# Performance work log

Hardware: AMD Instinct MI355X
Metric: run time of the kernel (lower is better)

Reference implementation:

```python
import jax, jax.numpy as jnp
import numpy as np

N_NODES = 50000
N_EDGES = 1600000
N_EDGE_F = 128
GLOBAL_F = 64
N_GRAPHS = 512
HIDDEN = N_EDGE_F // 2


def setup_inputs() -> dict:
    key = jax.random.key(0)
    k = jax.random.split(key, 8)
    x = jax.random.normal(k[0], (N_NODES, N_EDGE_F), dtype=jnp.float32)
    edge_index = jax.random.randint(k[1], (2, N_EDGES), 0, N_NODES, dtype=jnp.int64)
    edge_attr = jax.random.normal(k[2], (N_EDGES, N_EDGE_F), dtype=jnp.float32)
    u = jax.random.normal(k[3], (N_GRAPHS, GLOBAL_F), dtype=jnp.float32)
    batch = jnp.sort(jax.random.randint(k[4], (N_NODES,), 0, N_GRAPHS, dtype=jnp.int64))
    # MLP params (Linear1: in=n_edge_f+global_f, out=hidden; Linear2: hidden -> global_f)
    in1 = N_EDGE_F + GLOBAL_F
    W1 = jax.random.normal(k[5], (in1, HIDDEN), dtype=jnp.float32) / np.sqrt(in1)
    b1 = jnp.zeros((HIDDEN,), dtype=jnp.float32)
    W2 = jax.random.normal(k[6], (HIDDEN, GLOBAL_F), dtype=jnp.float32) / np.sqrt(HIDDEN)
    b2 = jnp.zeros((GLOBAL_F,), dtype=jnp.float32)
    return {"x": x, "edge_index": edge_index, "edge_attr": edge_attr, "u": u,
            "batch": batch, "W1": W1, "b1": b1, "W2": W2, "b2": b2}


def reference(x, edge_index, edge_attr, u, batch, W1, b1, W2, b2):
    # graph id of each edge = graph id of its source node
    seg = batch[edge_index[0]]                                   # [E]
    sums = jax.ops.segment_sum(edge_attr, seg, num_segments=N_GRAPHS)  # [B, n_edge_f]
    counts = jax.ops.segment_sum(jnp.ones((edge_attr.shape[0],), edge_attr.dtype),
                                 seg, num_segments=N_GRAPHS)
    mean = sums / jnp.maximum(counts, 1.0)[:, None]              # scatter-mean (0 for empty)
    out = jnp.concatenate([u, mean], axis=1)                     # [B, global_f + n_edge_f]
    # dropout in eval mode == identity
    h = jax.nn.relu(out @ W1 + b1)
    return h @ W2 + b2
```

## Files before the change

kernel.cpp:

```cpp
#include <hip/hip_runtime.h>
#include <hip/hip_bf16.h>

using u32 = unsigned int;
using u16 = unsigned short;

#define NGR   512
#define NF    128
#define GF    64
#define HID   64
#define IN1   192
#define SPLIT 8

#define HT    256
#define ITEMS 10
#define EPB   (HT * ITEMS)

__global__ void zero_counts_kernel(u32* __restrict__ counts) {
    counts[threadIdx.x] = 0u;
}

__global__ void hist_kernel(const int* __restrict__ ei0,
                            const int* __restrict__ batch,
                            u32* __restrict__ g_counts,
                            u16* __restrict__ seg, int E) {
    __shared__ u32 h[NGR];
    int tid = threadIdx.x;
    h[tid] = 0u; h[tid + 256] = 0u;
    __syncthreads();
    int base = blockIdx.x * EPB + tid;
#pragma unroll
    for (int i = 0; i < ITEMS; ++i) {
        int e = base + i * HT;
        if (e < E) {
            int s = batch[ei0[e]];
            seg[e] = (u16)s;
            atomicAdd(&h[s], 1u);
        }
    }
    __syncthreads();
    u32 v0 = h[tid];       if (v0) atomicAdd(&g_counts[tid], v0);
    u32 v1 = h[tid + 256]; if (v1) atomicAdd(&g_counts[tid + 256], v1);
}

__global__ void scan_kernel(const u32* __restrict__ counts,
                            u32* __restrict__ offsets,
                            u32* __restrict__ cursor) {
    __shared__ u32 A[NGR], B[NGR];
    int t = threadIdx.x;
    u32 c = counts[t];
    A[t] = c;
    __syncthreads();
    u32* src = A; u32* dst = B;
    for (int off = 1; off < NGR; off <<= 1) {
        u32 v = src[t];
        if (t >= off) v += src[t - off];
        dst[t] = v;
        __syncthreads();
        u32* tmp = src; src = dst; dst = tmp;
    }
    u32 exc = src[t] - c;
    offsets[t] = exc;
    cursor[t]  = exc;
}

__global__ void scatter_kernel(const u16* __restrict__ seg,
                               u32* __restrict__ cursor,
                               u32* __restrict__ sorted, int E) {
    __shared__ u32 h[NGR];
    __shared__ u32 bs[NGR];
    int tid = threadIdx.x;
    h[tid] = 0u; h[tid + 256] = 0u;
    __syncthreads();
    int base = blockIdx.x * EPB + tid;
    u16 segs[ITEMS];
    u16 ranks[ITEMS];
#pragma unroll
    for (int i = 0; i < ITEMS; ++i) {
        int e = base + i * HT;
        if (e < E) {
            int s = seg[e];
            segs[i]  = (u16)s;
            ranks[i] = (u16)atomicAdd(&h[s], 1u);
        }
    }
    __syncthreads();
    u32 v0 = h[tid];       if (v0) bs[tid]       = atomicAdd(&cursor[tid], v0);
    u32 v1 = h[tid + 256]; if (v1) bs[tid + 256] = atomicAdd(&cursor[tid + 256], v1);
    __syncthreads();
#pragma unroll
    for (int i = 0; i < ITEMS; ++i) {
        int e = base + i * HT;
        if (e < E) {
            sorted[bs[segs[i]] + ranks[i]] = (u32)e;
        }
    }
}

__launch_bounds__(256, 8)
__global__ void reduce_kernel(const float* __restrict__ edge_attr,
                              const u32* __restrict__ sorted,
                              const u32* __restrict__ counts,
                              const u32* __restrict__ offsets,
                              float* __restrict__ partial) {
    __shared__ float red[8 * NF];
    int tid = threadIdx.x;
    int g   = blockIdx.x >> 3;
    int s   = blockIdx.x & (SPLIT - 1);
    u32 off = offsets[g];
    u32 cnt = counts[g];
    u32 chunk = (cnt + SPLIT - 1) / SPLIT;
    u32 start = (u32)s * chunk;
    u32 end   = min(cnt, start + chunk);

    int row  = tid >> 5;
    int lane = tid & 31;

    float4 a0 = make_float4(0.f, 0.f, 0.f, 0.f);
    float4 a1 = a0, a2 = a0, a3 = a0;

    u32 j = start + (u32)row;
    for (; j + 24 < end; j += 32) {
        u32 e0 = sorted[off + j];
        u32 e1 = sorted[off + j + 8];
        u32 e2 = sorted[off + j + 16];
        u32 e3 = sorted[off + j + 24];
        float4 v0 = ((const float4*)(edge_attr + (size_t)e0 * NF))[lane];
        float4 v1 = ((const float4*)(edge_attr + (size_t)e1 * NF))[lane];
        float4 v2 = ((const float4*)(edge_attr + (size_t)e2 * NF))[lane];
        float4 v3 = ((const float4*)(edge_attr + (size_t)e3 * NF))[lane];
        a0.x += v0.x; a0.y += v0.y; a0.z += v0.z; a0.w += v0.w;
        a1.x += v1.x; a1.y += v1.y; a1.z += v1.z; a1.w += v1.w;
        a2.x += v2.x; a2.y += v2.y; a2.z += v2.z; a2.w += v2.w;
        a3.x += v3.x; a3.y += v3.y; a3.z += v3.z; a3.w += v3.w;
    }
    for (; j < end; j += 8) {
        u32 e = sorted[off + j];
        float4 v = ((const float4*)(edge_attr + (size_t)e * NF))[lane];
        a0.x += v.x; a0.y += v.y; a0.z += v.z; a0.w += v.w;
    }
    a0.x += a1.x + a2.x + a3.x;
    a0.y += a1.y + a2.y + a3.y;
    a0.z += a1.z + a2.z + a3.z;
    a0.w += a1.w + a2.w + a3.w;
    ((float4*)red)[row * 32 + lane] = a0;
    __syncthreads();

    if (tid < NF) {
        float v = 0.f;
#pragma unroll
        for (int r = 0; r < 8; ++r) v += red[r * NF + tid];
        partial[(size_t)blockIdx.x * NF + tid] = v;
    }
}

__global__ void final_kernel(const float* __restrict__ partial,
                             const u32* __restrict__ counts,
                             const float* __restrict__ u,
                             const float* __restrict__ W1,
                             const float* __restrict__ b1,
                             const float* __restrict__ W2,
                             const float* __restrict__ b2,
                             float* __restrict__ out) {
    __shared__ float vin[IN1];
    __shared__ float hv[HID];
    int b = blockIdx.x, t = threadIdx.x;
    if (t < NF) {
        float s = 0.f;
#pragma unroll
        for (int r = 0; r < SPLIT; ++r)
            s += partial[(size_t)(b * SPLIT + r) * NF + t];
        vin[GF + t] = s / fmaxf((float)counts[b], 1.0f);
    }
    if (t < GF) vin[t] = u[b * GF + t];
    __syncthreads();
    if (t < HID) {
        float acc = b1[t];
#pragma unroll
        for (int k = 0; k < IN1; ++k) acc += vin[k] * W1[k * HID + t];
        hv[t] = fmaxf(acc, 0.0f);
    }
    __syncthreads();
    if (t < GF) {
        float acc = b2[t];
#pragma unroll
        for (int k = 0; k < HID; ++k) acc += hv[k] * W2[k * GF + t];
        out[b * GF + t] = acc;
    }
}

extern "C" void kernel_launch(void* const* d_in, const int* in_sizes, int n_in,
                              void* d_out, int out_size, void* d_ws, size_t ws_size,
                              hipStream_t stream) {
    const int*   ei        = (const int*)d_in[1];
    const float* edge_attr = (const float*)d_in[2];
    const float* u         = (const float*)d_in[3];
    const int*   batch     = (const int*)d_in[4];
    const float* W1        = (const float*)d_in[5];
    const float* b1        = (const float*)d_in[6];
    const float* W2        = (const float*)d_in[7];
    const float* b2        = (const float*)d_in[8];
    float*       out       = (float*)d_out;

    const int E = in_sizes[1] / 2;
    const int* ei0 = ei;

    u32*   sorted  = (u32*)d_ws;
    float* partial = (float*)(sorted + E);
    u32*   counts  = (u32*)(partial + (size_t)NGR * SPLIT * NF);
    u32*   offsets = counts + NGR;
    u32*   cursor  = offsets + NGR;
    u16*   seg     = (u16*)(cursor + NGR);

    const int nblocks = (E + EPB - 1) / EPB;

    zero_counts_kernel<<<1, NGR, 0, stream>>>(counts);
    hist_kernel<<<nblocks, HT, 0, stream>>>(ei0, batch, counts, seg, E);
    scan_kernel<<<1, NGR, 0, stream>>>(counts, offsets, cursor);
    scatter_kernel<<<nblocks, HT, 0, stream>>>(seg, cursor, sorted, E);
    reduce_kernel<<<NGR * SPLIT, 256, 0, stream>>>(edge_attr, sorted, counts,
                                                   offsets, partial);
    final_kernel<<<NGR, 128, 0, stream>>>(partial, counts, u, W1, b1, W2, b2, out);
}
```

Measured before the change: 214.0 us.

## Balance reduce work with fixed-size chunk work list and nontemporal loads

Replaces the fixed 8-way split per graph with a work list built in the scan kernel, where each item covers up to 1024 sorted edges. The reduce grid is a fixed-size launch that exits early past the item count, and the final kernel sums a variable number of partials per graph. Edge attribute loads become nontemporal vector loads so the streamed rows do not pollute cache. This aims to balance load across blocks, since graph sizes vary. The cost is a serial work-list write in the scan kernel and a hard MAXIT cap that could overflow if there are many items.

```diff
diff --git a/kernel.cpp b/kernel.cpp
--- a/kernel.cpp
+++ b/kernel.cpp
@@ -1,15 +1,17 @@
 #include <hip/hip_runtime.h>
 #include <hip/hip_bf16.h>
 
-using u32 = unsigned int;
-using u16 = unsigned short;
+typedef unsigned int u32;
+typedef unsigned short u16;
+typedef float f32x4 __attribute__((ext_vector_type(4)));
 
 #define NGR   512
 #define NF    128
 #define GF    64
 #define HID   64
 #define IN1   192
-#define SPLIT 8
+#define CHUNK 1024
+#define MAXIT 2600
 
 #define HT    256
 #define ITEMS 10
@@ -44,13 +46,16 @@
 
 __global__ void scan_kernel(const u32* __restrict__ counts,
                             u32* __restrict__ offsets,
-                            u32* __restrict__ cursor) {
+                            u32* __restrict__ cursor,
+                            u32* __restrict__ work,
+                            u32* __restrict__ item_start,
+                            u32* __restrict__ header) {
     __shared__ u32 A[NGR], B[NGR];
     int t = threadIdx.x;
     u32 c = counts[t];
     A[t] = c;
     __syncthreads();
-    u32* src = A; u32* dst = B;
+    u32 *src = A, *dst = B;
     for (int off = 1; off < NGR; off <<= 1) {
         u32 v = src[t];
         if (t >= off) v += src[t - off];
@@ -61,6 +66,22 @@
     u32 exc = src[t] - c;
     offsets[t] = exc;
     cursor[t]  = exc;
+    __syncthreads();
+    u32 ns = (c + CHUNK - 1) / CHUNK;
+    A[t] = ns;
+    __syncthreads();
+    src = A; dst = B;
+    for (int off = 1; off < NGR; off <<= 1) {
+        u32 v = src[t];
+        if (t >= off) v += src[t - off];
+        dst[t] = v;
+        __syncthreads();
+        u32* tmp = src; src = dst; dst = tmp;
+    }
+    u32 istart = src[t] - ns;
+    item_start[t] = istart;
+    if (t == NGR - 1) { item_start[NGR] = istart + ns; header[0] = istart + ns; }
+    for (u32 s = 0; s < ns; ++s) work[istart + s] = ((u32)t << 16) | s;
 }
 
 __global__ void scatter_kernel(const u16* __restrict__ seg,
@@ -90,9 +111,7 @@
 #pragma unroll
     for (int i = 0; i < ITEMS; ++i) {
         int e = base + i * HT;
-        if (e < E) {
-            sorted[bs[segs[i]] + ranks[i]] = (u32)e;
-        }
+        if (e < E) sorted[bs[segs[i]] + ranks[i]] = (u32)e;
     }
 }
 
@@ -101,60 +120,57 @@
                               const u32* __restrict__ sorted,
                               const u32* __restrict__ counts,
                               const u32* __restrict__ offsets,
+                              const u32* __restrict__ work,
+                              const u32* __restrict__ header,
                               float* __restrict__ partial) {
+    const u32 id = blockIdx.x;
+    if (id >= header[0]) return;
     __shared__ float red[8 * NF];
-    int tid = threadIdx.x;
-    int g   = blockIdx.x >> 3;
-    int s   = blockIdx.x & (SPLIT - 1);
-    u32 off = offsets[g];
-    u32 cnt = counts[g];
-    u32 chunk = (cnt + SPLIT - 1) / SPLIT;
-    u32 start = (u32)s * chunk;
-    u32 end   = min(cnt, start + chunk);
-
-    int row  = tid >> 5;
-    int lane = tid & 31;
-
-    float4 a0 = make_float4(0.f, 0.f, 0.f, 0.f);
-    float4 a1 = a0, a2 = a0, a3 = a0;
-
-    u32 j = start + (u32)row;
-    for (; j + 24 < end; j += 32) {
+
+    const u32 w = work[id];
+    const int g = (int)(w >> 16);
+    const u32 sl = w & 0xFFFFu;
+    const u32 off = offsets[g] + sl * CHUNK;
+    const u32 len = min((u32)CHUNK, counts[g] - sl * CHUNK);
+
+    const int tid = threadIdx.x;
+    const int row = tid >> 5;
+    const int lane = tid & 31;
+
+    f32x4 a0 = {0.f,0.f,0.f,0.f}, a1 = a0, a2 = a0, a3 = a0;
+
+    u32 j = (u32)row;
+    for (; j + 24 < len; j += 32) {
         u32 e0 = sorted[off + j];
         u32 e1 = sorted[off + j + 8];
         u32 e2 = sorted[off + j + 16];
         u32 e3 = sorted[off + j + 24];
-        float4 v0 = ((const float4*)(edge_attr + (size_t)e0 * NF))[lane];
-        float4 v1 = ((const float4*)(edge_attr + (size_t)e1 * NF))[lane];
-        float4 v2 = ((const float4*)(edge_attr + (size_t)e2 * NF))[lane];
-        float4 v3 = ((const float4*)(edge_attr + (size_t)e3 * NF))[lane];
-        a0.x += v0.x; a0.y += v0.y; a0.z += v0.z; a0.w += v0.w;
-        a1.x += v1.x; a1.y += v1.y; a1.z += v1.z; a1.w += v1.w;
-        a2.x += v2.x; a2.y += v2.y; a2.z += v2.z; a2.w += v2.w;
-        a3.x += v3.x; a3.y += v3.y; a3.z += v3.z; a3.w += v3.w;
-    }
-    for (; j < end; j += 8) {
+        f32x4 v0 = __builtin_nontemporal_load((const f32x4*)(edge_attr + (size_t)e0 * NF) + lane);
+        f32x4 v1 = __builtin_nontemporal_load((const f32x4*)(edge_attr + (size_t)e1 * NF) + lane);
+        f32x4 v2 = __builtin_nontemporal_load((const f32x4*)(edge_attr + (size_t)e2 * NF) + lane);
+        f32x4 v3 = __builtin_nontemporal_load((const f32x4*)(edge_attr + (size_t)e3 * NF) + lane);
+        a0 += v0; a1 += v1; a2 += v2; a3 += v3;
+    }
+    for (; j < len; j += 8) {
         u32 e = sorted[off + j];
-        float4 v = ((const float4*)(edge_attr + (size_t)e * NF))[lane];
-        a0.x += v.x; a0.y += v.y; a0.z += v.z; a0.w += v.w;
-    }
-    a0.x += a1.x + a2.x + a3.x;
-    a0.y += a1.y + a2.y + a3.y;
-    a0.z += a1.z + a2.z + a3.z;
-    a0.w += a1.w + a2.w + a3.w;
-    ((float4*)red)[row * 32 + lane] = a0;
+        f32x4 v = __builtin_nontemporal_load((const f32x4*)(edge_attr + (size_t)e * NF) + lane);
+        a0 += v;
+    }
+    a0 += a1 + a2 + a3;
+    *(f32x4*)(red + row * NF + lane * 4) = a0;
     __syncthreads();
 
     if (tid < NF) {
-        float v = 0.f;
-#pragma unroll
-        for (int r = 0; r < 8; ++r) v += red[r * NF + tid];
-        partial[(size_t)blockIdx.x * NF + tid] = v;
+        float s = 0.f;
+#pragma unroll
+        for (int r = 0; r < 8; ++r) s += red[r * NF + tid];
+        partial[(size_t)id * NF + tid] = s;
     }
 }
 
 __global__ void final_kernel(const float* __restrict__ partial,
                              const u32* __restrict__ counts,
+                             const u32* __restrict__ item_start,
                              const float* __restrict__ u,
                              const float* __restrict__ W1,
                              const float* __restrict__ b1,
@@ -163,15 +179,14 @@
                              float* __restrict__ out) {
     __shared__ float vin[IN1];
     __shared__ float hv[HID];
-    int b = blockIdx.x, t = threadIdx.x;
+    const int g = blockIdx.x, t = threadIdx.x;
+    const u32 a = item_start[g], b = item_start[g + 1];
     if (t < NF) {
         float s = 0.f;
-#pragma unroll
-        for (int r = 0; r < SPLIT; ++r)
-            s += partial[(size_t)(b * SPLIT + r) * NF + t];
-        vin[GF + t] = s / fmaxf((float)counts[b], 1.0f);
-    }
-    if (t < GF) vin[t] = u[b * GF + t];
+        for (u32 it = a; it < b; ++it) s += partial[(size_t)it * NF + t];
+        vin[GF + t] = s / fmaxf((float)counts[g], 1.0f);
+    }
+    if (t >= NF && t < NF + GF) vin[t - NF] = u[g * GF + (t - NF)];
     __syncthreads();
     if (t < HID) {
         float acc = b1[t];
@@ -184,7 +199,7 @@
         float acc = b2[t];
 #pragma unroll
         for (int k = 0; k < HID; ++k) acc += hv[k] * W2[k * GF + t];
-        out[b * GF + t] = acc;
+        out[g * GF + t] = acc;
     }
 }
 
@@ -204,20 +219,24 @@
     const int E = in_sizes[1] / 2;
     const int* ei0 = ei;
 
-    u32*   sorted  = (u32*)d_ws;
-    float* partial = (float*)(sorted + E);
-    u32*   counts  = (u32*)(partial + (size_t)NGR * SPLIT * NF);
-    u32*   offsets = counts + NGR;
-    u32*   cursor  = offsets + NGR;
-    u16*   seg     = (u16*)(cursor + NGR);
+    u32*   sorted     = (u32*)d_ws;
+    float* partial    = (float*)(sorted + E);
+    u32*   counts     = (u32*)(partial + (size_t)MAXIT * NF);
+    u32*   offsets    = counts + NGR;
+    u32*   cursor     = offsets + NGR;
+    u32*   item_start = cursor + NGR;
+    u32*   header     = item_start + NGR + 1;
+    u32*   work       = header + 16;
+    u16*   seg        = (u16*)(work + MAXIT);
 
     const int nblocks = (E + EPB - 1) / EPB;
 
     zero_counts_kernel<<<1, NGR, 0, stream>>>(counts);
     hist_kernel<<<nblocks, HT, 0, stream>>>(ei0, batch, counts, seg, E);
-    scan_kernel<<<1, NGR, 0, stream>>>(counts, offsets, cursor);
+    scan_kernel<<<1, NGR, 0, stream>>>(counts, offsets, cursor, work, item_start, header);
     scatter_kernel<<<nblocks, HT, 0, stream>>>(seg, cursor, sorted, E);
-    reduce_kernel<<<NGR * SPLIT, 256, 0, stream>>>(edge_attr, sorted, counts,
-                                                   offsets, partial);
-    final_kernel<<<NGR, 128, 0, stream>>>(partial, counts, u, W1, b1, W2, b2, out);
-}
+    reduce_kernel<<<MAXIT, 256, 0, stream>>>(edge_attr, sorted, counts, offsets,
+                                             work, header, partial);
+    final_kernel<<<NGR, 256, 0, stream>>>(partial, counts, item_start,
+                                          u, W1, b1, W2, b2, out);
+}
```

New measurement: 208.5 us. 2.6% less time.
